# Kernel tuning notes

Measured on AMD Instinct MI355X. Metric: run time of the kernel, lower is better.

The kernel has to match this reference:

```python
import jax, jax.numpy as jnp
import numpy as np
import math

E, Z, L, B, MAXPOS = 1024, 256, 2048, 8, 2048
EPS = 1e-5

def setup_inputs() -> dict:
    rng = jax.random.key(0)
    ks = jax.random.split(rng, 12)
    s = 0.02  # bert init std
    return dict(
        query=jax.random.normal(ks[0], (L, B, E), jnp.float32),
        key_in=jax.random.normal(ks[1], (L, B, E), jnp.float32),
        value=jax.random.normal(ks[2], (L, B, E), jnp.float32),
        ln_w=jnp.ones((E,), jnp.float32),
        ln_b=jnp.zeros((E,), jnp.float32),
        Wv=jax.random.normal(ks[3], (E, E), jnp.float32) * s,
        bv=jnp.zeros((E,), jnp.float32),
        Wk=jax.random.normal(ks[4], (Z, E), jnp.float32) * s,
        bk=jnp.zeros((Z,), jnp.float32),
        Wqru=jax.random.normal(ks[5], (2 * E + Z, E), jnp.float32) * s,
        bqru=jnp.zeros((2 * E + Z,), jnp.float32),
        Wh=jax.random.normal(ks[6], (E, E), jnp.float32) * s,
        bh=jnp.zeros((E,), jnp.float32),
        gamma=jax.random.normal(ks[7], (2, Z), jnp.float32) * 0.02,
        beta=jax.random.normal(ks[8], (2, Z), jnp.float32) * 0.02,
        relpos=jax.random.normal(ks[9], (2 * MAXPOS - 1,), jnp.float32) * 0.02,
    )

def _layernorm(x, w, b):
    mu = jnp.mean(x, axis=-1, keepdims=True)
    var = jnp.mean(jnp.square(x - mu), axis=-1, keepdims=True)
    return (x - mu) * jax.lax.rsqrt(var + EPS) * w + b

def _l2norm(x):
    # torch F.normalize: x / max(||x||, eps)
    n = jnp.sqrt(jnp.sum(jnp.square(x), axis=-1, keepdims=True))
    return x / jnp.maximum(n, EPS)

def _simple_rel_bias(relpos, slen, clen):
    # toeplitz bias: bias[i,j] = relpos[MAXPOS-1 + (j - i)]
    n = max(slen, clen)
    b = relpos[MAXPOS - n: MAXPOS + n - 1]  # [2n-1]
    idx = (jnp.arange(n)[None, :] - jnp.arange(n)[:, None]) + (n - 1)
    t = b[idx]  # [n, n]
    return t[:slen, :clen]

def reference(query, key_in, value, ln_w, ln_b, Wv, bv, Wk, bk, Wqru, bqru, Wh, bh, gamma, beta, relpos):
    # query/key_in/value: [T, B, E]
    slen, clen = query.shape[0], key_in.shape[0]
    nq = _layernorm(query, ln_w, ln_b)
    g = gamma + 1.0
    base = jnp.einsum('sbe,fe->sbf', nq, Wqru) + bqru  # [T,B,2E+Z]
    q, u, r = base[..., :Z], base[..., Z:Z + E], base[..., Z + E:]
    q = _l2norm(q) * g[0] + beta[0]          # [T,B,Z]
    u = jax.nn.sigmoid(u)                    # [T,B,E]
    r = jax.nn.silu(r)                       # [T,B,E]
    k = jnp.einsum('cbe,ze->cbz', key_in, Wk) + bk
    k = _l2norm(k) * g[1] + beta[1]          # [C,B,Z]
    v = jax.nn.silu(jnp.einsum('cbe,fe->cbf', value, Wv) + bv)  # [C,B,E]
    len_scale = 1.0 / math.sqrt(clen)
    bias = _simple_rel_bias(relpos, slen, clen)  # [T,C]
    qk = jnp.einsum('sbz,cbz->bsc', q, k) * len_scale + bias
    attn = jnp.square(jax.nn.relu(qk))  # relu2 activation, [B,T,C]
    h = jnp.einsum('bsc,cbe->sbe', attn, v)  # [T,B,E]
    h = jnp.einsum('sbe,fe->sbf', h * r, Wh) + bh
    out = query + u * (h - query)  # addcmul gating
    return out
```

## Files before the change

kernel.cpp:

```cpp
#include <hip/hip_runtime.h>
#include <cstdint>


#define EN 1024
#define ZN 256
#define LN_ 2048
#define BN_ 8
#define MROWS (LN_ * BN_)
#define QRU_N (2 * EN + ZN)
#define LEN_SCALE 0.022097086912079608f

typedef unsigned short u16;
typedef __bf16 bf16x8 __attribute__((ext_vector_type(8)));
typedef float f32x4 __attribute__((ext_vector_type(4)));

__device__ __forceinline__ u16 f2bf(float f) {
    unsigned int u = __float_as_uint(f);
    u = (u + 0x7fff + ((u >> 16) & 1)) >> 16;
    return (u16)u;
}
__device__ __forceinline__ float bf2f(u16 s) {
    return __uint_as_float(((unsigned int)s) << 16);
}
__device__ __forceinline__ void store_bf16x4(u16* p, float a, float b, float c, float d) {
    union { u16 h[4]; uint2 v; } pk;
    pk.h[0] = f2bf(a); pk.h[1] = f2bf(b); pk.h[2] = f2bf(c); pk.h[3] = f2bf(d);
    *(uint2*)p = pk.v;
}

__device__ __forceinline__ void async_load16(const void* g, void* l) {
    __builtin_amdgcn_global_load_lds(
        (const __attribute__((address_space(1))) void*)g,
        (__attribute__((address_space(3))) void*)l,
        16, 0, 0);
}

template <typename Epi>
__global__ __launch_bounds__(256, 4)
void gemm_bt(const u16* __restrict__ A, const u16* __restrict__ B,
             long long batchStrideA, long long batchStrideB, int K, Epi epi)
{
    __shared__ __align__(16) u16 As[128 * 64];
    __shared__ __align__(16) u16 Bs[128 * 64];

    const int tid  = threadIdx.x;
    const int lane = tid & 63;
    const int w    = tid >> 6;
    const int wm   = w >> 1, wn = w & 1;
    const int bz   = blockIdx.z;

    const int gx   = gridDim.x;
    const int nwg  = gx * gridDim.y;
    const int orig = blockIdx.y * gx + blockIdx.x;
    const int swz  = ((nwg & 7) == 0) ? ((orig & 7) * (nwg >> 3) + (orig >> 3)) : orig;
    const long long m0 = (long long)(swz / gx) * 128;
    const long long n0 = (long long)(swz % gx) * 128;

    const u16* Ab = A + bz * batchStrideA;
    const u16* Bb = B + bz * batchStrideB;

    const int srow = lane >> 3;
    const int scol = ((lane & 7) ^ srow) * 8;
    const int quad = lane >> 4;
    const int l16  = lane & 15;

    const int choff0 = ((quad     ^ (l16 & 7)) * 8);
    const int choff1 = (((4 + quad) ^ (l16 & 7)) * 8);

    const f32x4 fzero = {0.f, 0.f, 0.f, 0.f};
    f32x4 acc[4][4];
#pragma unroll
    for (int i = 0; i < 4; ++i)
#pragma unroll
        for (int j = 0; j < 4; ++j) acc[i][j] = fzero;

    for (int k0 = 0; k0 < K; k0 += 64) {
        __syncthreads();
#pragma unroll
        for (int t = 0; t < 4; ++t) {
            const int rbase = w * 32 + t * 8;
            async_load16(Ab + (m0 + rbase + srow) * K + (k0 + scol), (void*)&As[rbase * 64]);
            async_load16(Bb + (n0 + rbase + srow) * K + (k0 + scol), (void*)&Bs[rbase * 64]);
        }
        __builtin_amdgcn_s_waitcnt(0);
        __syncthreads();

#pragma unroll
        for (int h = 0; h < 2; ++h) {
            const int ch = h ? choff1 : choff0;
            bf16x8 af[4], bfv[4];
#pragma unroll
            for (int mi = 0; mi < 4; ++mi)
                af[mi] = *(const bf16x8*)&As[(wm * 64 + mi * 16 + l16) * 64 + ch];
#pragma unroll
            for (int ni = 0; ni < 4; ++ni)
                bfv[ni] = *(const bf16x8*)&Bs[(wn * 64 + ni * 16 + l16) * 64 + ch];
#pragma unroll
            for (int mi = 0; mi < 4; ++mi)
#pragma unroll
                for (int ni = 0; ni < 4; ++ni)
                    acc[mi][ni] = __builtin_amdgcn_mfma_f32_16x16x32_bf16(
                        af[mi], bfv[ni], acc[mi][ni], 0, 0, 0);
        }
    }

#pragma unroll
    for (int mi = 0; mi < 4; ++mi)
#pragma unroll
        for (int ni = 0; ni < 4; ++ni)
#pragma unroll
            for (int r = 0; r < 4; ++r) {
                int m = (int)m0 + wm * 64 + mi * 16 + quad * 4 + r;
                int n = (int)n0 + wn * 64 + ni * 16 + l16;
                epi(bz, m, n, acc[mi][ni][r]);
            }
}

struct EpiRaw {
    float* out; const float* bias;
    __device__ void operator()(int, int m, int n, float v) const {
        out[(long long)m * ZN + n] = v + bias[n];
    }
};
struct EpiQru {
    float* qraw; u16* u; u16* r; const float* bqru;
    __device__ void operator()(int, int m, int n, float v) const {
        v += bqru[n];
        if (n < ZN) {
            qraw[(long long)m * ZN + n] = v;
        } else if (n < ZN + EN) {
            float s = 1.f / (1.f + __expf(-v));
            u[(long long)m * EN + (n - ZN)] = f2bf(s);
        } else {
            float s = v / (1.f + __expf(-v));
            r[(long long)m * EN + (n - ZN - EN)] = f2bf(s);
        }
    }
};
struct EpiV {
    u16* v; const float* bv;
    __device__ void operator()(int, int m, int n, float acc) const {
        float x = acc + bv[n];
        float s = x / (1.f + __expf(-x));
        int b = m & 7, c = m >> 3;
        v[((long long)b * LN_ + c) * EN + n] = f2bf(s);
    }
};
struct EpiQK {
    u16* attn; const float* relpos;
    __device__ void operator()(int bz, int m, int n, float v) const {
        float val = v * LEN_SCALE + relpos[2047 + n - m];
        float t = fmaxf(val, 0.f);
        attn[(long long)bz * LN_ * LN_ + (long long)m * LN_ + n] = f2bf(t * t);
    }
};
struct EpiH {
    u16* hr; const u16* r;
    __device__ void operator()(int bz, int m, int n, float acc) const {
        long long idx = ((long long)m * BN_ + bz) * EN + n;
        hr[idx] = f2bf(acc * bf2f(r[idx]));
    }
};
struct EpiOut {
    float* out; const float* query; const u16* u; const float* bh;
    __device__ void operator()(int, int m, int n, float acc) const {
        long long idx = (long long)m * EN + n;
        float qv = query[idx];
        float uu = bf2f(u[idx]);
        out[idx] = qv + uu * ((acc + bh[n]) - qv);
    }
};

__global__ __launch_bounds__(256)
void prep_kernel(const float* __restrict__ query, const float* __restrict__ key_in,
                 const float* __restrict__ value, const float* __restrict__ ln_w,
                 const float* __restrict__ ln_b,
                 u16* __restrict__ nq, u16* __restrict__ kin, u16* __restrict__ val)
{
    const int w = threadIdx.x >> 6, lane = threadIdx.x & 63;
    const int m = blockIdx.x * 4 + w;
    const long long rowb = (long long)m * EN;

    float4 q[4];
    float a1 = 0.f, a2 = 0.f;
#pragma unroll
    for (int p = 0; p < 4; ++p) {
        q[p] = *(const float4*)(query + rowb + p * 256 + lane * 4);
        a1 += q[p].x + q[p].y + q[p].z + q[p].w;
        a2 += q[p].x * q[p].x + q[p].y * q[p].y + q[p].z * q[p].z + q[p].w * q[p].w;
    }
#pragma unroll
    for (int o = 32; o; o >>= 1) { a1 += __shfl_down(a1, o, 64); a2 += __shfl_down(a2, o, 64); }
    const float S1 = __shfl(a1, 0, 64);
    const float S2 = __shfl(a2, 0, 64);
    const float mu = S1 * (1.f / EN);
    const float var = S2 * (1.f / EN) - mu * mu;
    const float rstd = rsqrtf(var + 1e-5f);

#pragma unroll
    for (int p = 0; p < 4; ++p) {
        const long long off = rowb + p * 256 + lane * 4;
        const int e = p * 256 + lane * 4;
        float4 wv = *(const float4*)(ln_w + e);
        float4 bv = *(const float4*)(ln_b + e);
        store_bf16x4(nq + off,
                     (q[p].x - mu) * rstd * wv.x + bv.x, (q[p].y - mu) * rstd * wv.y + bv.y,
                     (q[p].z - mu) * rstd * wv.z + bv.z, (q[p].w - mu) * rstd * wv.w + bv.w);
        float4 kq = *(const float4*)(key_in + off);
        store_bf16x4(kin + off, kq.x, kq.y, kq.z, kq.w);
        float4 vq = *(const float4*)(value + off);
        store_bf16x4(val + off, vq.x, vq.y, vq.z, vq.w);
    }
}

__global__ __launch_bounds__(256)
void l2norm_both(const float* __restrict__ kraw, const float* __restrict__ qraw,
                 u16* __restrict__ kb, u16* __restrict__ qb,
                 const float* __restrict__ gamma, const float* __restrict__ beta)
{
    __shared__ float red[4];
    const int m = blockIdx.x, z = threadIdx.x;
    const int which = blockIdx.y;
    const float* raw = which ? qraw : kraw;
    u16* out = which ? qb : kb;
    const float* g = gamma + (which ? 0 : ZN);
    const float* be = beta + (which ? 0 : ZN);
    const float x = raw[(long long)m * ZN + z];
    float ss = x * x;
#pragma unroll
    for (int o = 32; o; o >>= 1) ss += __shfl_down(ss, o, 64);
    if ((z & 63) == 0) red[z >> 6] = ss;
    __syncthreads();
    const float tot = red[0] + red[1] + red[2] + red[3];
    const float inv = 1.f / fmaxf(sqrtf(tot), 1e-5f);
    const float res = x * inv * (g[z] + 1.f) + be[z];
    const int b = m & 7, s = m >> 3;
    out[((long long)b * LN_ + s) * ZN + z] = f2bf(res);
}

__global__ __launch_bounds__(256)
void transpose_bc(const u16* __restrict__ v, u16* __restrict__ vT)
{
    __shared__ u16 tile[64][65];
    const int b = blockIdx.z;
    const int c0 = blockIdx.y * 64, e0 = blockIdx.x * 64;
    const int t  = threadIdx.x;
    const int rc = t >> 3;
    const int ec = t & 7;
    const u16* src = v + (long long)b * LN_ * EN;
    u16* dst = vT + (long long)b * EN * LN_;

#pragma unroll
    for (int i = 0; i < 64; i += 32) {
        union { uint4 v4; u16 h[8]; } ld;
        ld.v4 = *(const uint4*)(src + (long long)(c0 + rc + i) * EN + (e0 + ec * 8));
#pragma unroll
        for (int j = 0; j < 8; ++j) tile[rc + i][ec * 8 + j] = ld.h[j];
    }
    __syncthreads();
#pragma unroll
    for (int i = 0; i < 64; i += 32) {
        union { uint4 v4; u16 h[8]; } st;
#pragma unroll
        for (int j = 0; j < 8; ++j) st.h[j] = tile[ec * 8 + j][rc + i];
        *(uint4*)(dst + (long long)(e0 + rc + i) * LN_ + (c0 + ec * 8)) = st.v4;
    }
}

#define N4_QRU (QRU_N * EN / 4)
#define N4_K   (ZN * EN / 4)
#define N4_V   (EN * EN / 4)
#define N4_H   (EN * EN / 4)
#define N4_TOT (N4_QRU + N4_K + N4_V + N4_H)

__global__ __launch_bounds__(256)
void castw_all(const float* __restrict__ Wqru, const float* __restrict__ Wk,
               const float* __restrict__ Wv,   const float* __restrict__ Wh,
               u16* __restrict__ dQru, u16* __restrict__ dK,
               u16* __restrict__ dV,   u16* __restrict__ dH)
{
    int i = blockIdx.x * 256 + threadIdx.x;
    if (i >= N4_TOT) return;
    const float* src; u16* dst; int j = i;
    if (j < N4_QRU)                { src = Wqru; dst = dQru; }
    else if ((j -= N4_QRU) < N4_K) { src = Wk;   dst = dK;   }
    else if ((j -= N4_K) < N4_V)   { src = Wv;   dst = dV;   }
    else { j -= N4_V;                src = Wh;   dst = dH;   }
    float4 x = ((const float4*)src)[j];
    store_bf16x4(dst + (long long)j * 4, x.x, x.y, x.z, x.w);
}

extern "C" void kernel_launch(void* const* d_in, const int* in_sizes, int n_in,
                              void* d_out, int out_size, void* d_ws, size_t ws_size,
                              hipStream_t stream)
{
    const float* query  = (const float*)d_in[0];
    const float* key_in = (const float*)d_in[1];
    const float* value  = (const float*)d_in[2];
    const float* ln_w   = (const float*)d_in[3];
    const float* ln_b   = (const float*)d_in[4];
    const float* Wv     = (const float*)d_in[5];
    const float* bv     = (const float*)d_in[6];
    const float* Wk     = (const float*)d_in[7];
    const float* bk     = (const float*)d_in[8];
    const float* Wqru   = (const float*)d_in[9];
    const float* bqru   = (const float*)d_in[10];
    const float* Wh     = (const float*)d_in[11];
    const float* bh     = (const float*)d_in[12];
    const float* gamma  = (const float*)d_in[13];
    const float* beta   = (const float*)d_in[14];
    const float* relpos = (const float*)d_in[15];
    float* out = (float*)d_out;

    char* ws = (char*)d_ws;
    const size_t MB = 1ull << 20;
    u16*   nq    = (u16*)(ws + 0);
    u16*   kin   = (u16*)(ws + 32 * MB);
    float* qraw  = (float*)(ws + 32 * MB);
    u16*   vbce  = (u16*)(ws + 32 * MB);
    u16*   attn  = (u16*)(ws + 0);
    u16*   valb  = (u16*)(ws + 64 * MB);
    u16*   hr    = (u16*)(ws + 64 * MB);
    u16*   qb    = (u16*)(ws + 96 * MB);
    u16*   kb    = (u16*)(ws + 104 * MB);
    u16*   ub    = (u16*)(ws + 112 * MB);
    u16*   rb    = (u16*)(ws + 144 * MB);
    u16*   vT    = (u16*)(ws + 176 * MB);
    float* kraw  = (float*)(ws + 208 * MB);
    u16*   WqruB = (u16*)(ws + 224 * MB);
    u16*   WkB   = (u16*)(ws + 229 * MB);
    u16*   WvB   = (u16*)(ws + 230 * MB);
    u16*   WhB   = (u16*)(ws + 232 * MB);
    (void)ws_size; (void)in_sizes; (void)n_in; (void)out_size;

    castw_all<<<dim3((N4_TOT + 255) / 256), 256, 0, stream>>>(
        Wqru, Wk, Wv, Wh, WqruB, WkB, WvB, WhB);

    prep_kernel<<<dim3(MROWS / 4), 256, 0, stream>>>(query, key_in, value, ln_w, ln_b, nq, kin, valb);

    gemm_bt<<<dim3(ZN / 128, MROWS / 128, 1), 256, 0, stream>>>(
        kin, WkB, 0LL, 0LL, EN, EpiRaw{kraw, bk});

    gemm_bt<<<dim3(QRU_N / 128, MROWS / 128, 1), 256, 0, stream>>>(
        nq, WqruB, 0LL, 0LL, EN, EpiQru{qraw, ub, rb, bqru});

    l2norm_both<<<dim3(MROWS, 2), 256, 0, stream>>>(kraw, qraw, kb, qb, gamma, beta);

    gemm_bt<<<dim3(EN / 128, MROWS / 128, 1), 256, 0, stream>>>(
        valb, WvB, 0LL, 0LL, EN, EpiV{vbce, bv});
    transpose_bc<<<dim3(EN / 64, LN_ / 64, BN_), 256, 0, stream>>>(vbce, vT);

    gemm_bt<<<dim3(LN_ / 128, LN_ / 128, BN_), 256, 0, stream>>>(
        qb, kb, (long long)LN_ * ZN, (long long)LN_ * ZN, ZN, EpiQK{attn, relpos});

    gemm_bt<<<dim3(EN / 128, LN_ / 128, BN_), 256, 0, stream>>>(
        attn, vT, (long long)LN_ * LN_, (long long)EN * LN_, LN_, EpiH{hr, rb});

    gemm_bt<<<dim3(EN / 128, MROWS / 128, 1), 256, 0, stream>>>(
        hr, WhB, 0LL, 0LL, EN, EpiOut{out, query, ub, bh});
}
```

Baseline: 678.5 us.

## Merge independent launches into grouped kernels: pre, fused projection GEMMs, post

Combines the weight cast and layernorm/cast prep into one launch, runs the three input-projection GEMMs (QRU, K, V) as a single grouped launch with per-segment epilogues, and merges the l2norm and V transpose into one launch. The workspace layout is reshuffled so the merged kernels' buffers no longer alias. The aim is to cut launch gaps and tail underutilisation between small dependent-free kernels. The cost is branchier kernels and more register pressure from the three inlined epilogues.

```diff
diff --git a/kernel.cpp b/kernel.cpp
--- a/kernel.cpp
+++ b/kernel.cpp
@@ -35,6 +35,130 @@
         16, 0, 0);
 }
 
+#define GEMM_CORE(Ab, Bb, m0, n0, K)                                             \
+    for (int k0 = 0; k0 < (K); k0 += 64) {                                       \
+        __syncthreads();                                                         \
+        _Pragma("unroll")                                                        \
+        for (int t = 0; t < 4; ++t) {                                            \
+            const int rbase = w * 32 + t * 8;                                    \
+            async_load16((Ab) + ((m0) + rbase + srow) * (K) + (k0 + scol),       \
+                         (void*)&As[rbase * 64]);                                \
+            async_load16((Bb) + ((n0) + rbase + srow) * (K) + (k0 + scol),       \
+                         (void*)&Bs[rbase * 64]);                                \
+        }                                                                        \
+        __builtin_amdgcn_s_waitcnt(0);                                           \
+        __syncthreads();                                                         \
+        _Pragma("unroll")                                                        \
+        for (int h = 0; h < 2; ++h) {                                            \
+            const int ch = h ? choff1 : choff0;                                  \
+            bf16x8 af[4], bfv[4];                                                \
+            _Pragma("unroll")                                                    \
+            for (int mi = 0; mi < 4; ++mi)                                       \
+                af[mi] = *(const bf16x8*)&As[(wm * 64 + mi * 16 + l16) * 64 + ch];\
+            _Pragma("unroll")                                                    \
+            for (int ni = 0; ni < 4; ++ni)                                       \
+                bfv[ni] = *(const bf16x8*)&Bs[(wn * 64 + ni * 16 + l16) * 64 + ch];\
+            _Pragma("unroll")                                                    \
+            for (int mi = 0; mi < 4; ++mi)                                       \
+                _Pragma("unroll")                                                \
+                for (int ni = 0; ni < 4; ++ni)                                   \
+                    acc[mi][ni] = __builtin_amdgcn_mfma_f32_16x16x32_bf16(       \
+                        af[mi], bfv[ni], acc[mi][ni], 0, 0, 0);                  \
+        }                                                                        \
+    }
+
+#define GEMM_PREAMBLE()                                                          \
+    const int tid  = threadIdx.x;                                                \
+    const int lane = tid & 63;                                                   \
+    const int w    = tid >> 6;                                                   \
+    const int wm   = w >> 1, wn = w & 1;                                         \
+    const int srow = lane >> 3;                                                  \
+    const int scol = ((lane & 7) ^ srow) * 8;                                    \
+    const int quad = lane >> 4;                                                  \
+    const int l16  = lane & 15;                                                  \
+    const int choff0 = ((quad     ^ (l16 & 7)) * 8);                             \
+    const int choff1 = (((4 + quad) ^ (l16 & 7)) * 8);                           \
+    const f32x4 fzero = {0.f, 0.f, 0.f, 0.f};                                    \
+    f32x4 acc[4][4];                                                             \
+    _Pragma("unroll")                                                            \
+    for (int i = 0; i < 4; ++i)                                                  \
+        _Pragma("unroll")                                                        \
+        for (int j = 0; j < 4; ++j) acc[i][j] = fzero;
+
+__global__ __launch_bounds__(256, 4)
+void gemm_fused3(const u16* __restrict__ nq, const u16* __restrict__ kin,
+                 const u16* __restrict__ valb,
+                 const u16* __restrict__ Wqru, const u16* __restrict__ Wk,
+                 const u16* __restrict__ Wv,
+                 float* __restrict__ qraw, u16* __restrict__ ub, u16* __restrict__ rb,
+                 const float* __restrict__ bqru,
+                 float* __restrict__ kraw, const float* __restrict__ bk,
+                 u16* __restrict__ vbce, const float* __restrict__ bv)
+{
+    __shared__ __align__(16) u16 As[128 * 64];
+    __shared__ __align__(16) u16 Bs[128 * 64];
+
+    const int id = blockIdx.x;
+    int seg, local, gx, nwg;
+    const u16 *A, *B;
+    if (id < 2304)      { seg = 0; local = id;        gx = 18; nwg = 2304; A = nq;   B = Wqru; }
+    else if (id < 2560) { seg = 1; local = id - 2304; gx = 2;  nwg = 256;  A = kin;  B = Wk;  }
+    else                { seg = 2; local = id - 2560; gx = 8;  nwg = 1024; A = valb; B = Wv;  }
+    const int swz = (local & 7) * (nwg >> 3) + (local >> 3);
+    const long long m0 = (long long)(swz / gx) * 128;
+    const long long n0 = (long long)(swz % gx) * 128;
+
+    GEMM_PREAMBLE();
+    GEMM_CORE(A, B, m0, n0, 1024);
+
+    if (seg == 0) {
+#pragma unroll
+        for (int mi = 0; mi < 4; ++mi)
+#pragma unroll
+            for (int ni = 0; ni < 4; ++ni)
+#pragma unroll
+                for (int r = 0; r < 4; ++r) {
+                    int m = (int)m0 + wm * 64 + mi * 16 + quad * 4 + r;
+                    int n = (int)n0 + wn * 64 + ni * 16 + l16;
+                    float v = acc[mi][ni][r] + bqru[n];
+                    if (n < ZN) {
+                        qraw[(long long)m * ZN + n] = v;
+                    } else if (n < ZN + EN) {
+                        float s = 1.f / (1.f + __expf(-v));
+                        ub[(long long)m * EN + (n - ZN)] = f2bf(s);
+                    } else {
+                        float s = v / (1.f + __expf(-v));
+                        rb[(long long)m * EN + (n - ZN - EN)] = f2bf(s);
+                    }
+                }
+    } else if (seg == 1) {
+#pragma unroll
+        for (int mi = 0; mi < 4; ++mi)
+#pragma unroll
+            for (int ni = 0; ni < 4; ++ni)
+#pragma unroll
+                for (int r = 0; r < 4; ++r) {
+                    int m = (int)m0 + wm * 64 + mi * 16 + quad * 4 + r;
+                    int n = (int)n0 + wn * 64 + ni * 16 + l16;
+                    kraw[(long long)m * ZN + n] = acc[mi][ni][r] + bk[n];
+                }
+    } else {
+#pragma unroll
+        for (int mi = 0; mi < 4; ++mi)
+#pragma unroll
+            for (int ni = 0; ni < 4; ++ni)
+#pragma unroll
+                for (int r = 0; r < 4; ++r) {
+                    int m = (int)m0 + wm * 64 + mi * 16 + quad * 4 + r;
+                    int n = (int)n0 + wn * 64 + ni * 16 + l16;
+                    float x = acc[mi][ni][r] + bv[n];
+                    float s = x / (1.f + __expf(-x));
+                    int b = m & 7, c = m >> 3;
+                    vbce[((long long)b * LN_ + c) * EN + n] = f2bf(s);
+                }
+    }
+}
+
 template <typename Epi>
 __global__ __launch_bounds__(256, 4)
 void gemm_bt(const u16* __restrict__ A, const u16* __restrict__ B,
@@ -43,12 +167,7 @@
     __shared__ __align__(16) u16 As[128 * 64];
     __shared__ __align__(16) u16 Bs[128 * 64];
 
-    const int tid  = threadIdx.x;
-    const int lane = tid & 63;
-    const int w    = tid >> 6;
-    const int wm   = w >> 1, wn = w & 1;
     const int bz   = blockIdx.z;
-
     const int gx   = gridDim.x;
     const int nwg  = gx * gridDim.y;
     const int orig = blockIdx.y * gx + blockIdx.x;
@@ -59,50 +178,8 @@
     const u16* Ab = A + bz * batchStrideA;
     const u16* Bb = B + bz * batchStrideB;
 
-    const int srow = lane >> 3;
-    const int scol = ((lane & 7) ^ srow) * 8;
-    const int quad = lane >> 4;
-    const int l16  = lane & 15;
-
-    const int choff0 = ((quad     ^ (l16 & 7)) * 8);
-    const int choff1 = (((4 + quad) ^ (l16 & 7)) * 8);
-
-    const f32x4 fzero = {0.f, 0.f, 0.f, 0.f};
-    f32x4 acc[4][4];
-#pragma unroll
-    for (int i = 0; i < 4; ++i)
-#pragma unroll
-        for (int j = 0; j < 4; ++j) acc[i][j] = fzero;
-
-    for (int k0 = 0; k0 < K; k0 += 64) {
-        __syncthreads();
-#pragma unroll
-        for (int t = 0; t < 4; ++t) {
-            const int rbase = w * 32 + t * 8;
-            async_load16(Ab + (m0 + rbase + srow) * K + (k0 + scol), (void*)&As[rbase * 64]);
-            async_load16(Bb + (n0 + rbase + srow) * K + (k0 + scol), (void*)&Bs[rbase * 64]);
-        }
-        __builtin_amdgcn_s_waitcnt(0);
-        __syncthreads();
-
-#pragma unroll
-        for (int h = 0; h < 2; ++h) {
-            const int ch = h ? choff1 : choff0;
-            bf16x8 af[4], bfv[4];
-#pragma unroll
-            for (int mi = 0; mi < 4; ++mi)
-                af[mi] = *(const bf16x8*)&As[(wm * 64 + mi * 16 + l16) * 64 + ch];
-#pragma unroll
-            for (int ni = 0; ni < 4; ++ni)
-                bfv[ni] = *(const bf16x8*)&Bs[(wn * 64 + ni * 16 + l16) * 64 + ch];
-#pragma unroll
-            for (int mi = 0; mi < 4; ++mi)
-#pragma unroll
-                for (int ni = 0; ni < 4; ++ni)
-                    acc[mi][ni] = __builtin_amdgcn_mfma_f32_16x16x32_bf16(
-                        af[mi], bfv[ni], acc[mi][ni], 0, 0, 0);
-        }
-    }
+    GEMM_PREAMBLE();
+    GEMM_CORE(Ab, Bb, m0, n0, K);
 
 #pragma unroll
     for (int mi = 0; mi < 4; ++mi)
@@ -116,36 +193,6 @@
             }
 }
 
-struct EpiRaw {
-    float* out; const float* bias;
-    __device__ void operator()(int, int m, int n, float v) const {
-        out[(long long)m * ZN + n] = v + bias[n];
-    }
-};
-struct EpiQru {
-    float* qraw; u16* u; u16* r; const float* bqru;
-    __device__ void operator()(int, int m, int n, float v) const {
-        v += bqru[n];
-        if (n < ZN) {
-            qraw[(long long)m * ZN + n] = v;
-        } else if (n < ZN + EN) {
-            float s = 1.f / (1.f + __expf(-v));
-            u[(long long)m * EN + (n - ZN)] = f2bf(s);
-        } else {
-            float s = v / (1.f + __expf(-v));
-            r[(long long)m * EN + (n - ZN - EN)] = f2bf(s);
-        }
-    }
-};
-struct EpiV {
-    u16* v; const float* bv;
-    __device__ void operator()(int, int m, int n, float acc) const {
-        float x = acc + bv[n];
-        float s = x / (1.f + __expf(-x));
-        int b = m & 7, c = m >> 3;
-        v[((long long)b * LN_ + c) * EN + n] = f2bf(s);
-    }
-};
 struct EpiQK {
     u16* attn; const float* relpos;
     __device__ void operator()(int bz, int m, int n, float v) const {
@@ -171,123 +218,126 @@
     }
 };
 
-__global__ __launch_bounds__(256)
-void prep_kernel(const float* __restrict__ query, const float* __restrict__ key_in,
-                 const float* __restrict__ value, const float* __restrict__ ln_w,
-                 const float* __restrict__ ln_b,
-                 u16* __restrict__ nq, u16* __restrict__ kin, u16* __restrict__ val)
-{
-    const int w = threadIdx.x >> 6, lane = threadIdx.x & 63;
-    const int m = blockIdx.x * 4 + w;
-    const long long rowb = (long long)m * EN;
-
-    float4 q[4];
-    float a1 = 0.f, a2 = 0.f;
-#pragma unroll
-    for (int p = 0; p < 4; ++p) {
-        q[p] = *(const float4*)(query + rowb + p * 256 + lane * 4);
-        a1 += q[p].x + q[p].y + q[p].z + q[p].w;
-        a2 += q[p].x * q[p].x + q[p].y * q[p].y + q[p].z * q[p].z + q[p].w * q[p].w;
-    }
-#pragma unroll
-    for (int o = 32; o; o >>= 1) { a1 += __shfl_down(a1, o, 64); a2 += __shfl_down(a2, o, 64); }
-    const float S1 = __shfl(a1, 0, 64);
-    const float S2 = __shfl(a2, 0, 64);
-    const float mu = S1 * (1.f / EN);
-    const float var = S2 * (1.f / EN) - mu * mu;
-    const float rstd = rsqrtf(var + 1e-5f);
-
-#pragma unroll
-    for (int p = 0; p < 4; ++p) {
-        const long long off = rowb + p * 256 + lane * 4;
-        const int e = p * 256 + lane * 4;
-        float4 wv = *(const float4*)(ln_w + e);
-        float4 bv = *(const float4*)(ln_b + e);
-        store_bf16x4(nq + off,
-                     (q[p].x - mu) * rstd * wv.x + bv.x, (q[p].y - mu) * rstd * wv.y + bv.y,
-                     (q[p].z - mu) * rstd * wv.z + bv.z, (q[p].w - mu) * rstd * wv.w + bv.w);
-        float4 kq = *(const float4*)(key_in + off);
-        store_bf16x4(kin + off, kq.x, kq.y, kq.z, kq.w);
-        float4 vq = *(const float4*)(value + off);
-        store_bf16x4(val + off, vq.x, vq.y, vq.z, vq.w);
-    }
-}
-
-__global__ __launch_bounds__(256)
-void l2norm_both(const float* __restrict__ kraw, const float* __restrict__ qraw,
-                 u16* __restrict__ kb, u16* __restrict__ qb,
-                 const float* __restrict__ gamma, const float* __restrict__ beta)
-{
-    __shared__ float red[4];
-    const int m = blockIdx.x, z = threadIdx.x;
-    const int which = blockIdx.y;
-    const float* raw = which ? qraw : kraw;
-    u16* out = which ? qb : kb;
-    const float* g = gamma + (which ? 0 : ZN);
-    const float* be = beta + (which ? 0 : ZN);
-    const float x = raw[(long long)m * ZN + z];
-    float ss = x * x;
-#pragma unroll
-    for (int o = 32; o; o >>= 1) ss += __shfl_down(ss, o, 64);
-    if ((z & 63) == 0) red[z >> 6] = ss;
-    __syncthreads();
-    const float tot = red[0] + red[1] + red[2] + red[3];
-    const float inv = 1.f / fmaxf(sqrtf(tot), 1e-5f);
-    const float res = x * inv * (g[z] + 1.f) + be[z];
-    const int b = m & 7, s = m >> 3;
-    out[((long long)b * LN_ + s) * ZN + z] = f2bf(res);
-}
-
-__global__ __launch_bounds__(256)
-void transpose_bc(const u16* __restrict__ v, u16* __restrict__ vT)
-{
-    __shared__ u16 tile[64][65];
-    const int b = blockIdx.z;
-    const int c0 = blockIdx.y * 64, e0 = blockIdx.x * 64;
-    const int t  = threadIdx.x;
-    const int rc = t >> 3;
-    const int ec = t & 7;
-    const u16* src = v + (long long)b * LN_ * EN;
-    u16* dst = vT + (long long)b * EN * LN_;
-
-#pragma unroll
-    for (int i = 0; i < 64; i += 32) {
-        union { uint4 v4; u16 h[8]; } ld;
-        ld.v4 = *(const uint4*)(src + (long long)(c0 + rc + i) * EN + (e0 + ec * 8));
-#pragma unroll
-        for (int j = 0; j < 8; ++j) tile[rc + i][ec * 8 + j] = ld.h[j];
-    }
-    __syncthreads();
-#pragma unroll
-    for (int i = 0; i < 64; i += 32) {
-        union { uint4 v4; u16 h[8]; } st;
-#pragma unroll
-        for (int j = 0; j < 8; ++j) st.h[j] = tile[ec * 8 + j][rc + i];
-        *(uint4*)(dst + (long long)(e0 + rc + i) * LN_ + (c0 + ec * 8)) = st.v4;
-    }
-}
-
 #define N4_QRU (QRU_N * EN / 4)
 #define N4_K   (ZN * EN / 4)
 #define N4_V   (EN * EN / 4)
 #define N4_H   (EN * EN / 4)
 #define N4_TOT (N4_QRU + N4_K + N4_V + N4_H)
+#define PREP_BLKS (MROWS / 4)
+#define CAST_BLKS (N4_TOT / 256)
 
 __global__ __launch_bounds__(256)
-void castw_all(const float* __restrict__ Wqru, const float* __restrict__ Wk,
-               const float* __restrict__ Wv,   const float* __restrict__ Wh,
-               u16* __restrict__ dQru, u16* __restrict__ dK,
-               u16* __restrict__ dV,   u16* __restrict__ dH)
+void pre_kernel(const float* __restrict__ query, const float* __restrict__ key_in,
+                const float* __restrict__ value, const float* __restrict__ ln_w,
+                const float* __restrict__ ln_b,
+                u16* __restrict__ nq, u16* __restrict__ kin, u16* __restrict__ val,
+                const float* __restrict__ Wqru, const float* __restrict__ Wk,
+                const float* __restrict__ Wv,   const float* __restrict__ Wh,
+                u16* __restrict__ dQru, u16* __restrict__ dK,
+                u16* __restrict__ dV,   u16* __restrict__ dH)
 {
-    int i = blockIdx.x * 256 + threadIdx.x;
-    if (i >= N4_TOT) return;
-    const float* src; u16* dst; int j = i;
-    if (j < N4_QRU)                { src = Wqru; dst = dQru; }
-    else if ((j -= N4_QRU) < N4_K) { src = Wk;   dst = dK;   }
-    else if ((j -= N4_K) < N4_V)   { src = Wv;   dst = dV;   }
-    else { j -= N4_V;                src = Wh;   dst = dH;   }
-    float4 x = ((const float4*)src)[j];
-    store_bf16x4(dst + (long long)j * 4, x.x, x.y, x.z, x.w);
+    const int id = blockIdx.x;
+    if (id < PREP_BLKS) {
+        const int w = threadIdx.x >> 6, lane = threadIdx.x & 63;
+        const int m = id * 4 + w;
+        const long long rowb = (long long)m * EN;
+        float4 q[4];
+        float a1 = 0.f, a2 = 0.f;
+#pragma unroll
+        for (int p = 0; p < 4; ++p) {
+            q[p] = *(const float4*)(query + rowb + p * 256 + lane * 4);
+            a1 += q[p].x + q[p].y + q[p].z + q[p].w;
+            a2 += q[p].x * q[p].x + q[p].y * q[p].y + q[p].z * q[p].z + q[p].w * q[p].w;
+        }
+#pragma unroll
+        for (int o = 32; o; o >>= 1) { a1 += __shfl_down(a1, o, 64); a2 += __shfl_down(a2, o, 64); }
+        const float S1 = __shfl(a1, 0, 64);
+        const float S2 = __shfl(a2, 0, 64);
+        const float mu = S1 * (1.f / EN);
+        const float var = S2 * (1.f / EN) - mu * mu;
+        const float rstd = rsqrtf(var + 1e-5f);
+#pragma unroll
+        for (int p = 0; p < 4; ++p) {
+            const long long off = rowb + p * 256 + lane * 4;
+            const int e = p * 256 + lane * 4;
+            float4 wv = *(const float4*)(ln_w + e);
+            float4 bvv = *(const float4*)(ln_b + e);
+            store_bf16x4(nq + off,
+                         (q[p].x - mu) * rstd * wv.x + bvv.x, (q[p].y - mu) * rstd * wv.y + bvv.y,
+                         (q[p].z - mu) * rstd * wv.z + bvv.z, (q[p].w - mu) * rstd * wv.w + bvv.w);
+            float4 kq = *(const float4*)(key_in + off);
+            store_bf16x4(kin + off, kq.x, kq.y, kq.z, kq.w);
+            float4 vq = *(const float4*)(value + off);
+            store_bf16x4(val + off, vq.x, vq.y, vq.z, vq.w);
+        }
+    } else {
+        int i = (id - PREP_BLKS) * 256 + threadIdx.x;
+        const float* src; u16* dst; int j = i;
+        if (j < N4_QRU)                { src = Wqru; dst = dQru; }
+        else if ((j -= N4_QRU) < N4_K) { src = Wk;   dst = dK;   }
+        else if ((j -= N4_K) < N4_V)   { src = Wv;   dst = dV;   }
+        else { j -= N4_V;                src = Wh;   dst = dH;   }
+        float4 x = ((const float4*)src)[j];
+        store_bf16x4(dst + (long long)j * 4, x.x, x.y, x.z, x.w);
+    }
+}
+
+#define L2_BLKS (2 * MROWS)
+#define TR_BLKS (BN_ * (LN_ / 64) * (EN / 64))
+
+__global__ __launch_bounds__(256)
+void post_kernel(const float* __restrict__ kraw, const float* __restrict__ qraw,
+                 u16* __restrict__ kb, u16* __restrict__ qb,
+                 const float* __restrict__ gamma, const float* __restrict__ beta,
+                 const u16* __restrict__ vbce, u16* __restrict__ vT)
+{
+    __shared__ u16 tile[64][65];
+    const int id = blockIdx.x;
+    if (id < L2_BLKS) {
+        float* red = (float*)&tile[0][0];
+        const int m = id & (MROWS - 1), z = threadIdx.x;
+        const int which = id >> 14;
+        const float* raw = which ? qraw : kraw;
+        u16* outp = which ? qb : kb;
+        const float* g = gamma + (which ? 0 : ZN);
+        const float* be = beta + (which ? 0 : ZN);
+        const float x = raw[(long long)m * ZN + z];
+        float ss = x * x;
+#pragma unroll
+        for (int o = 32; o; o >>= 1) ss += __shfl_down(ss, o, 64);
+        if ((z & 63) == 0) red[z >> 6] = ss;
+        __syncthreads();
+        const float tot = red[0] + red[1] + red[2] + red[3];
+        const float inv = 1.f / fmaxf(sqrtf(tot), 1e-5f);
+        const float res = x * inv * (g[z] + 1.f) + be[z];
+        const int b = m & 7, s = m >> 3;
+        outp[((long long)b * LN_ + s) * ZN + z] = f2bf(res);
+    } else {
+        const int id2 = id - L2_BLKS;
+        const int b  = id2 >> 9;
+        const int rem = id2 & 511;
+        const int e0 = (rem & 15) * 64, c0 = (rem >> 4) * 64;
+        const int t  = threadIdx.x;
+        const int rc = t >> 3;
+        const int ec = t & 7;
+        const u16* src = vbce + (long long)b * LN_ * EN;
+        u16* dst = vT + (long long)b * EN * LN_;
+#pragma unroll
+        for (int i = 0; i < 64; i += 32) {
+            union { uint4 v4; u16 h[8]; } ld;
+            ld.v4 = *(const uint4*)(src + (long long)(c0 + rc + i) * EN + (e0 + ec * 8));
+#pragma unroll
+            for (int j = 0; j < 8; ++j) tile[rc + i][ec * 8 + j] = ld.h[j];
+        }
+        __syncthreads();
+#pragma unroll
+        for (int i = 0; i < 64; i += 32) {
+            union { uint4 v4; u16 h[8]; } st;
+#pragma unroll
+            for (int j = 0; j < 8; ++j) st.h[j] = tile[ec * 8 + j][rc + i];
+            *(uint4*)(dst + (long long)(e0 + rc + i) * LN_ + (c0 + ec * 8)) = st.v4;
+        }
+    }
 }
 
 extern "C" void kernel_launch(void* const* d_in, const int* in_sizes, int n_in,
@@ -316,39 +366,33 @@
     const size_t MB = 1ull << 20;
     u16*   nq    = (u16*)(ws + 0);
     u16*   kin   = (u16*)(ws + 32 * MB);
-    float* qraw  = (float*)(ws + 32 * MB);
-    u16*   vbce  = (u16*)(ws + 32 * MB);
-    u16*   attn  = (u16*)(ws + 0);
     u16*   valb  = (u16*)(ws + 64 * MB);
-    u16*   hr    = (u16*)(ws + 64 * MB);
-    u16*   qb    = (u16*)(ws + 96 * MB);
-    u16*   kb    = (u16*)(ws + 104 * MB);
-    u16*   ub    = (u16*)(ws + 112 * MB);
-    u16*   rb    = (u16*)(ws + 144 * MB);
-    u16*   vT    = (u16*)(ws + 176 * MB);
-    float* kraw  = (float*)(ws + 208 * MB);
+    u16*   vbce  = (u16*)(ws + 96 * MB);
+    float* qraw  = (float*)(ws + 128 * MB);
+    float* kraw  = (float*)(ws + 144 * MB);
+    u16*   ub    = (u16*)(ws + 160 * MB);
+    u16*   rb    = (u16*)(ws + 192 * MB);
     u16*   WqruB = (u16*)(ws + 224 * MB);
     u16*   WkB   = (u16*)(ws + 229 * MB);
     u16*   WvB   = (u16*)(ws + 230 * MB);
     u16*   WhB   = (u16*)(ws + 232 * MB);
+    u16*   vT    = (u16*)(ws + 0);
+    u16*   qb    = (u16*)(ws + 32 * MB);
+    u16*   kb    = (u16*)(ws + 40 * MB);
+    u16*   attn  = (u16*)(ws + 48 * MB);
+    u16*   hr    = (u16*)(ws + 112 * MB);
     (void)ws_size; (void)in_sizes; (void)n_in; (void)out_size;
 
-    castw_all<<<dim3((N4_TOT + 255) / 256), 256, 0, stream>>>(
+    pre_kernel<<<dim3(PREP_BLKS + CAST_BLKS), 256, 0, stream>>>(
+        query, key_in, value, ln_w, ln_b, nq, kin, valb,
         Wqru, Wk, Wv, Wh, WqruB, WkB, WvB, WhB);
 
-    prep_kernel<<<dim3(MROWS / 4), 256, 0, stream>>>(query, key_in, value, ln_w, ln_b, nq, kin, valb);
-
-    gemm_bt<<<dim3(ZN / 128, MROWS / 128, 1), 256, 0, stream>>>(
-        kin, WkB, 0LL, 0LL, EN, EpiRaw{kraw, bk});
-
-    gemm_bt<<<dim3(QRU_N / 128, MROWS / 128, 1), 256, 0, stream>>>(
-        nq, WqruB, 0LL, 0LL, EN, EpiQru{qraw, ub, rb, bqru});
-
-    l2norm_both<<<dim3(MROWS, 2), 256, 0, stream>>>(kraw, qraw, kb, qb, gamma, beta);
-
-    gemm_bt<<<dim3(EN / 128, MROWS / 128, 1), 256, 0, stream>>>(
-        valb, WvB, 0LL, 0LL, EN, EpiV{vbce, bv});
-    transpose_bc<<<dim3(EN / 64, LN_ / 64, BN_), 256, 0, stream>>>(vbce, vT);
+    gemm_fused3<<<dim3(2304 + 256 + 1024), 256, 0, stream>>>(
+        nq, kin, valb, WqruB, WkB, WvB,
+        qraw, ub, rb, bqru, kraw, bk, vbce, bv);
+
+    post_kernel<<<dim3(L2_BLKS + TR_BLKS), 256, 0, stream>>>(
+        kraw, qraw, kb, qb, gamma, beta, vbce, vT);
 
     gemm_bt<<<dim3(LN_ / 128, LN_ / 128, BN_), 256, 0, stream>>>(
         qb, kb, (long long)LN_ * ZN, (long long)LN_ * ZN, ZN, EpiQK{attn, relpos});
```

Result: faster. 626.6 us (-7.7%).
